# Performance work log

Measured on AMD Instinct MI355X. Metric: run time of the kernel, lower is better.

The kernel has to match this reference:

```python
import jax, jax.numpy as jnp
import numpy as np

B, S, D = 4, 2048, 1024

def setup_inputs() -> dict:
    key = jax.random.key(0)
    ks = jax.random.split(key, 7)
    s = 1.0 / np.sqrt(D)
    return {
        "x":  jax.random.normal(ks[0], (B, S, D), dtype=jnp.float32),
        "Wq": jax.random.uniform(ks[1], (D, D), jnp.float32, -s, s),
        "bq": jax.random.uniform(ks[2], (D,),  jnp.float32, -s, s),
        "Wk": jax.random.uniform(ks[3], (D, D), jnp.float32, -s, s),
        "bk": jax.random.uniform(ks[4], (D,),  jnp.float32, -s, s),
        "Wv": jax.random.uniform(ks[5], (D, D), jnp.float32, -s, s),
        "bv": jax.random.uniform(ks[6], (D,),  jnp.float32, -s, s),
    }

def reference(x, Wq, bq, Wk, bk, Wv, bv):
    # Q/K/V projections: [B,S,D]
    Q = jnp.einsum('bsd,de->bse', x, Wq) + bq
    K = jnp.einsum('bsd,de->bse', x, Wk) + bk
    V = jnp.einsum('bsd,de->bse', x, Wv) + bv
    scale = 1.0 / jnp.sqrt(jnp.asarray(K.shape[-1], K.dtype))
    scores = jnp.einsum('bqd,bkd->bqk', Q, K) * scale  # [B,S,S]
    weights = jax.nn.softmax(scores, axis=-1)
    return jnp.einsum('bqk,bkd->bqd', weights, V)
```

## Files before the change

### kernel.cpp

```cpp
#include <hip/hip_runtime.h>

typedef __attribute__((ext_vector_type(4))) float f32x4;
typedef __attribute__((ext_vector_type(8))) short bf16x8;

__device__ __forceinline__ float bf2f(unsigned short u) {
  union { unsigned int i; float f; } x; x.i = ((unsigned int)u) << 16; return x.f;
}
__device__ __forceinline__ unsigned short f2bf(float f) {
  union { float f; unsigned int i; } x; x.f = f;
  unsigned int r = (x.i + 0x7FFFu + ((x.i >> 16) & 1u)) >> 16;
  return (unsigned short)r;
}

#define BARX __builtin_amdgcn_s_barrier()
#define LGK0 asm volatile("s_waitcnt lgkmcnt(0)" ::: "memory")
#define GLD(gsrc, ldsoff)                                                        \
  __builtin_amdgcn_global_load_lds(                                              \
      (const __attribute__((address_space(1))) void*)(gsrc),                     \
      (__attribute__((address_space(3))) void*)&lds[ldsoff], 16, 0, 0)

__global__ __launch_bounds__(256) void cvt_f2b(const float* __restrict__ src,
                                               unsigned short* __restrict__ dst, long n4) {
  long i = (long)blockIdx.x * 256 + threadIdx.x;
  long stride = (long)gridDim.x * 256;
  for (; i < n4; i += stride) {
    float4 v = *(const float4*)&src[i * 4];
    ushort4 o;
    o.x = f2bf(v.x); o.y = f2bf(v.y); o.z = f2bf(v.z); o.w = f2bf(v.w);
    *(ushort4*)&dst[i * 4] = o;
  }
}

__global__ __launch_bounds__(256) void transpose_f2b(const float* __restrict__ src,
                                                     unsigned short* __restrict__ dst,
                                                     int rows, int cols) {
  __shared__ float t[32][33];
  int bx = blockIdx.x * 32, by = blockIdx.y * 32;
  int tx = threadIdx.x, ty = threadIdx.y;
#pragma unroll
  for (int k = 0; k < 4; ++k)
    t[ty + 8 * k][tx] = src[(long)(by + ty + 8 * k) * cols + bx + tx];
  __syncthreads();
#pragma unroll
  for (int k = 0; k < 4; ++k)
    dst[(long)(bx + ty + 8 * k) * rows + by + tx] = f2bf(t[tx][ty + 8 * k]);
}

__global__ __launch_bounds__(256) void transpose_v(const unsigned short* __restrict__ src,
                                                   unsigned short* __restrict__ dst) {
  __shared__ unsigned short t[32][33];
  const long sb = (long)blockIdx.z * 2048 * 3072;
  const long db = (long)blockIdx.z * 1024 * 2048;
  int bx = blockIdx.x * 32, by = blockIdx.y * 32;
  int tx = threadIdx.x, ty = threadIdx.y;
#pragma unroll
  for (int k = 0; k < 4; ++k)
    t[ty + 8 * k][tx] = src[sb + (long)(by + ty + 8 * k) * 3072 + bx + tx];
  __syncthreads();
#pragma unroll
  for (int k = 0; k < 4; ++k)
    dst[db + (long)(bx + ty + 8 * k) * 2048 + by + tx] = t[tx][ty + 8 * k];
}

template <int MODE>
__global__ __launch_bounds__(512, 2) void gemm4p(const unsigned short* __restrict__ Ap,
                                                 const unsigned short* __restrict__ Bp,
                                                 void* __restrict__ Cv,
                                                 const float* __restrict__ q_,
                                                 const float* __restrict__ k_,
                                                 const float* __restrict__ v_,
                                                 int Kd, int lda, int ldb, int ldc, float scale,
                                                 long sA, long sB, long sC) {
  __shared__ unsigned short lds[65536];
  const int bz = blockIdx.z;
  Ap += (long)bz * sA; Bp += (long)bz * sB;
  const int tid = threadIdx.x;
  const int m0 = blockIdx.x * 256, n0 = blockIdx.y * 256;
  const int lane = tid & 63, wave = tid >> 6;
  const int wm = wave >> 2, wn = wave & 3;
  const int rr = tid >> 3;
  const int cSrc = ((tid & 7) ^ (rr & 7)) << 3;
  const int lc = lane & 15, lr = lane >> 4;
  const int x0 = (lc & 4) << 3;
  const int x1 = 32 ^ x0;
  const int klo = (lr << 3) ^ ((lc & 3) << 3);
  const int aoff = (wm * 128 + lc) * 64 + klo;
  const int boff = 16384 + (wn * 64 + lc) * 64 + klo;
  const int NT = Kd >> 6;

#define ST4(bufo, reg0, half, P, R0, ld, k0s)                                                    \
  {                                                                                              \
    _Pragma("unroll") for (int i_ = 0; i_ < 2; ++i_) {                                           \
      const unsigned short* g_ =                                                                 \
          (P) + (long)((R0) + (half) * 128 + i_ * 64 + rr) * (ld) + ((k0s) + cSrc);              \
      GLD(g_, (bufo) + (reg0) + (half) * 8192 + i_ * 4096 + tid * 8);                            \
    }                                                                                            \
  }

  f32x4 acc[8][4] = {};

  ST4(0, 16384, 0, Bp, n0, ldb, 0); ST4(0, 16384, 1, Bp, n0, ldb, 0);
  ST4(0, 0, 0, Ap, m0, lda, 0);     ST4(0, 0, 1, Ap, m0, lda, 0);
  ST4(32768, 16384, 0, Bp, n0, ldb, 64); ST4(32768, 16384, 1, Bp, n0, ldb, 64);
  ST4(32768, 0, 0, Ap, m0, lda, 64);     ST4(32768, 0, 1, Ap, m0, lda, 64);
  asm volatile("s_waitcnt vmcnt(8)" ::: "memory");
  BARX;

  for (int t = 0; t < NT; ++t) {
    const int bufo = (t & 1) << 15;
    const unsigned short* Lp = &lds[bufo];
    const int kn = (t + 2) << 6;
    const bool pf = (t + 2 < NT);
    bf16x8 a0[4][2], a1[4][2], b0[2][2], b1[2][2];
#pragma unroll
    for (int mi = 0; mi < 4; ++mi) {
      a0[mi][0] = *(const bf16x8*)&Lp[aoff + mi * 1024 + x0];
      a0[mi][1] = *(const bf16x8*)&Lp[aoff + mi * 1024 + x1];
    }
#pragma unroll
    for (int ni = 0; ni < 2; ++ni) {
      b0[ni][0] = *(const bf16x8*)&Lp[boff + ni * 1024 + x0];
      b0[ni][1] = *(const bf16x8*)&Lp[boff + ni * 1024 + x1];
    }
    BARX; LGK0;
    __builtin_amdgcn_s_setprio(1);
#pragma unroll
    for (int mi = 0; mi < 4; ++mi)
#pragma unroll
      for (int ni = 0; ni < 2; ++ni)
#pragma unroll
        for (int x = 0; x < 2; ++x)
          acc[mi][ni] = __builtin_amdgcn_mfma_f32_16x16x32_bf16(a0[mi][x], b0[ni][x], acc[mi][ni], 0, 0, 0);
    __builtin_amdgcn_s_setprio(0);
    BARX;
#pragma unroll
    for (int ni = 0; ni < 2; ++ni) {
      b1[ni][0] = *(const bf16x8*)&Lp[boff + 2048 + ni * 1024 + x0];
      b1[ni][1] = *(const bf16x8*)&Lp[boff + 2048 + ni * 1024 + x1];
    }
    BARX; LGK0;
    __builtin_amdgcn_s_setprio(1);
#pragma unroll
    for (int mi = 0; mi < 4; ++mi)
#pragma unroll
      for (int ni = 0; ni < 2; ++ni)
#pragma unroll
        for (int x = 0; x < 2; ++x)
          acc[mi][2 + ni] = __builtin_amdgcn_mfma_f32_16x16x32_bf16(a0[mi][x], b1[ni][x], acc[mi][2 + ni], 0, 0, 0);
    __builtin_amdgcn_s_setprio(0);
    BARX;
#pragma unroll
    for (int mi = 0; mi < 4; ++mi) {
      a1[mi][0] = *(const bf16x8*)&Lp[aoff + 4096 + mi * 1024 + x0];
      a1[mi][1] = *(const bf16x8*)&Lp[aoff + 4096 + mi * 1024 + x1];
    }
    if (pf) ST4(bufo, 16384, 0, Bp, n0, ldb, kn);
    BARX; LGK0;
    __builtin_amdgcn_s_setprio(1);
#pragma unroll
    for (int mi = 0; mi < 4; ++mi)
#pragma unroll
      for (int ni = 0; ni < 2; ++ni)
#pragma unroll
        for (int x = 0; x < 2; ++x)
          acc[4 + mi][2 + ni] = __builtin_amdgcn_mfma_f32_16x16x32_bf16(a1[mi][x], b1[ni][x], acc[4 + mi][2 + ni], 0, 0, 0);
    __builtin_amdgcn_s_setprio(0);
    BARX;
    if (pf) {
      ST4(bufo, 16384, 1, Bp, n0, ldb, kn);
      ST4(bufo, 0, 0, Ap, m0, lda, kn);
      ST4(bufo, 0, 1, Ap, m0, lda, kn);
    }
    BARX; LGK0;
    __builtin_amdgcn_s_setprio(1);
#pragma unroll
    for (int mi = 0; mi < 4; ++mi)
#pragma unroll
      for (int ni = 0; ni < 2; ++ni)
#pragma unroll
        for (int x = 0; x < 2; ++x)
          acc[4 + mi][ni] = __builtin_amdgcn_mfma_f32_16x16x32_bf16(a1[mi][x], b0[ni][x], acc[4 + mi][ni], 0, 0, 0);
    __builtin_amdgcn_s_setprio(0);
    if (pf) { asm volatile("s_waitcnt vmcnt(8)" ::: "memory"); }
    else    { asm volatile("s_waitcnt vmcnt(0)" ::: "memory"); }
    BARX;
  }
#undef ST4

  const int r0 = m0 + wm * 128 + lr * 4;
  const int c0 = n0 + wn * 64 + lc;
  unsigned short* C = (unsigned short*)Cv + (long)bz * sC;
#pragma unroll
  for (int nh = 0; nh < 2; ++nh)
#pragma unroll
    for (int ni = 0; ni < 2; ++ni) {
      const int col = c0 + nh * 32 + ni * 16;
      float bv = 0.0f;
      if (MODE == 0)
        bv = (col < 1024) ? q_[col] : ((col < 2048) ? k_[col - 1024] : v_[col - 2048]);
#pragma unroll
      for (int mh = 0; mh < 2; ++mh)
#pragma unroll
        for (int mi = 0; mi < 4; ++mi)
#pragma unroll
          for (int r = 0; r < 4; ++r) {
            float val = acc[mh * 4 + mi][nh * 2 + ni][r];
            val = (MODE == 0) ? (val + bv) : __expf(val * scale);
            C[(long)(r0 + mh * 64 + mi * 16 + r) * ldc + col] = f2bf(val);
          }
    }
}

__global__ __launch_bounds__(512, 2) void gemmpv(const unsigned short* __restrict__ Av,
                                                 const unsigned short* __restrict__ Bv,
                                                 float* __restrict__ Out,
                                                 const float* __restrict__ invden,
                                                 int Kd, int lda, int ldb, int ldc,
                                                 long sA, long sB, long sC) {
  __shared__ unsigned short lds[73728];
  const int bz = blockIdx.z;
  Av += (long)bz * sA; Bv += (long)bz * sB;
  const int tid = threadIdx.x;
  const int m0 = blockIdx.x * 128, n0 = blockIdx.y * 256;
  const int lane = tid & 63, wave = tid >> 6;
  const int wm = wave >> 2, wn = wave & 3;
  const int rr = tid >> 3;
  const int cSrc = ((tid & 7) ^ (rr & 7)) << 3;
  const int lc = lane & 15, lr = lane >> 4;
  const int x0 = (lc & 4) << 3;
  const int x1 = 32 ^ x0;
  const int klo = (lr << 3) ^ ((lc & 3) << 3);
  const int aoff = (wm * 64 + lc) * 64 + klo;
  const int boff = 8192 + (wn * 64 + lc) * 64 + klo;
  const int NT = Kd >> 6;

#define STA_PV(bufo, k0s)                                                                        \
  {                                                                                              \
    _Pragma("unroll") for (int i_ = 0; i_ < 2; ++i_) {                                           \
      const unsigned short* g_ = Av + (long)(m0 + i_ * 64 + rr) * lda + ((k0s) + cSrc);          \
      GLD(g_, (bufo) + i_ * 4096 + tid * 8);                                                     \
    }                                                                                            \
  }
#define STB_PV(bufo, k0s)                                                                        \
  {                                                                                              \
    _Pragma("unroll") for (int i_ = 0; i_ < 4; ++i_) {                                           \
      const unsigned short* g_ = Bv + (long)(n0 + i_ * 64 + rr) * ldb + ((k0s) + cSrc);          \
      GLD(g_, (bufo) + 8192 + i_ * 4096 + tid * 8);                                              \
    }                                                                                            \
  }

  f32x4 acc[4][4] = {};

  STB_PV(0, 0);      STA_PV(0, 0);
  STB_PV(24576, 64); STA_PV(24576, 64);
  asm volatile("s_waitcnt vmcnt(6)" ::: "memory");
  BARX;

  int cur = 0;
  for (int t = 0; t < NT; ++t) {
    const int stg = (cur >= 1) ? cur - 1 : 2;
    const unsigned short* Lp = &lds[cur * 24576];
    const int so = stg * 24576;
    const int kn = (t + 2) << 6;
    const bool pf = (t + 2 < NT);
    bf16x8 a0[2][2], a1[2][2], bb[2][2][2];
#pragma unroll
    for (int nh = 0; nh < 2; ++nh)
#pragma unroll
      for (int ni = 0; ni < 2; ++ni) {
        bb[nh][ni][0] = *(const bf16x8*)&Lp[boff + nh * 2048 + ni * 1024 + x0];
        bb[nh][ni][1] = *(const bf16x8*)&Lp[boff + nh * 2048 + ni * 1024 + x1];
      }
#pragma unroll
    for (int mi = 0; mi < 2; ++mi) {
      a0[mi][0] = *(const bf16x8*)&Lp[aoff + mi * 1024 + x0];
      a0[mi][1] = *(const bf16x8*)&Lp[aoff + mi * 1024 + x1];
    }
    if (pf) STB_PV(so, kn);
    BARX; LGK0;
    __builtin_amdgcn_s_setprio(1);
#pragma unroll
    for (int mi = 0; mi < 2; ++mi)
#pragma unroll
      for (int nh = 0; nh < 2; ++nh)
#pragma unroll
        for (int ni = 0; ni < 2; ++ni)
#pragma unroll
          for (int x = 0; x < 2; ++x)
            acc[mi][nh * 2 + ni] = __builtin_amdgcn_mfma_f32_16x16x32_bf16(
                a0[mi][x], bb[nh][ni][x], acc[mi][nh * 2 + ni], 0, 0, 0);
    __builtin_amdgcn_s_setprio(0);
    BARX;
#pragma unroll
    for (int mi = 0; mi < 2; ++mi) {
      a1[mi][0] = *(const bf16x8*)&Lp[aoff + 2048 + mi * 1024 + x0];
      a1[mi][1] = *(const bf16x8*)&Lp[aoff + 2048 + mi * 1024 + x1];
    }
    if (pf) STA_PV(so, kn);
    BARX; LGK0;
    __builtin_amdgcn_s_setprio(1);
#pragma unroll
    for (int mi = 0; mi < 2; ++mi)
#pragma unroll
      for (int nh = 0; nh < 2; ++nh)
#pragma unroll
        for (int ni = 0; ni < 2; ++ni)
#pragma unroll
          for (int x = 0; x < 2; ++x)
            acc[2 + mi][nh * 2 + ni] = __builtin_amdgcn_mfma_f32_16x16x32_bf16(
                a1[mi][x], bb[nh][ni][x], acc[2 + mi][nh * 2 + ni], 0, 0, 0);
    __builtin_amdgcn_s_setprio(0);
    if (pf) { asm volatile("s_waitcnt vmcnt(6)" ::: "memory"); }
    else    { asm volatile("s_waitcnt vmcnt(0)" ::: "memory"); }
    BARX;
    cur = (cur == 2) ? 0 : cur + 1;
  }
#undef STA_PV
#undef STB_PV

  const int r0 = m0 + wm * 64 + lr * 4;
  const int c0 = n0 + wn * 64 + lc;
  float* O = Out + (long)bz * sC;
  const float* idn = invden + (long)bz * 2048;
  float iv[2][2][4];
#pragma unroll
  for (int mh = 0; mh < 2; ++mh)
#pragma unroll
    for (int mi = 0; mi < 2; ++mi)
#pragma unroll
      for (int r = 0; r < 4; ++r)
        iv[mh][mi][r] = idn[r0 + mh * 32 + mi * 16 + r];
#pragma unroll
  for (int mh = 0; mh < 2; ++mh)
#pragma unroll
    for (int mi = 0; mi < 2; ++mi)
#pragma unroll
      for (int r = 0; r < 4; ++r) {
        const int row = r0 + mh * 32 + mi * 16 + r;
#pragma unroll
        for (int nh = 0; nh < 2; ++nh)
#pragma unroll
          for (int ni = 0; ni < 2; ++ni)
            O[(long)row * ldc + (c0 + nh * 32 + ni * 16)] =
                acc[mh * 2 + mi][nh * 2 + ni][r] * iv[mh][mi][r];
      }
}

__global__ __launch_bounds__(256) void rowsum_inv(const unsigned short* __restrict__ E,
                                                  float* __restrict__ invden) {
  const long row = blockIdx.x;
  const unsigned short* p = E + row * 2048;
  const int tid = threadIdx.x;
  const int lane = tid & 63, wave = tid >> 6;
  ushort4 h0 = *(const ushort4*)&p[tid * 8];
  ushort4 h1 = *(const ushort4*)&p[tid * 8 + 4];
  float s = bf2f(h0.x) + bf2f(h0.y) + bf2f(h0.z) + bf2f(h0.w) +
            bf2f(h1.x) + bf2f(h1.y) + bf2f(h1.z) + bf2f(h1.w);
#pragma unroll
  for (int o = 32; o >= 1; o >>= 1) s += __shfl_xor(s, o);
  __shared__ float ss[4];
  if (lane == 0) ss[wave] = s;
  __syncthreads();
  if (tid == 0) invden[row] = 1.0f / (ss[0] + ss[1] + ss[2] + ss[3]);
}

extern "C" void kernel_launch(void* const* d_in, const int* in_sizes, int n_in,
                              void* d_out, int out_size, void* d_ws, size_t ws_size,
                              hipStream_t stream) {
  const float* x  = (const float*)d_in[0];
  const float* Wq = (const float*)d_in[1];
  const float* bq = (const float*)d_in[2];
  const float* Wk = (const float*)d_in[3];
  const float* bk = (const float*)d_in[4];
  const float* Wv = (const float*)d_in[5];
  const float* bv = (const float*)d_in[6];
  float* out = (float*)d_out;

  const int Bb = 4, S = 2048, D = 1024;
  const long MS = (long)Bb * S;

  char* ws = (char*)d_ws;
  unsigned short* xb  = (unsigned short*)(ws);
  unsigned short* Wt  = (unsigned short*)(ws + (16L << 20));
  unsigned short* QKV = (unsigned short*)(ws + (22L << 20));
  unsigned short* Sc  = (unsigned short*)(ws + (70L << 20));
  unsigned short* VT  = xb;
  float* invden = (float*)(ws + (16L << 20));

  cvt_f2b<<<2048, 256, 0, stream>>>(x, xb, MS * D / 4);

  dim3 tb(32, 8);
  dim3 tg(D / 32, D / 32);
  transpose_f2b<<<tg, tb, 0, stream>>>(Wq, Wt, D, D);
  transpose_f2b<<<tg, tb, 0, stream>>>(Wk, Wt + 1024 * 1024, D, D);
  transpose_f2b<<<tg, tb, 0, stream>>>(Wv, Wt + 2 * 1024 * 1024, D, D);

  dim3 pgrid(MS / 256, 3072 / 256, 1);
  gemm4p<0><<<pgrid, 512, 0, stream>>>(xb, Wt, QKV, bq, bk, bv, D, D, D, 3072, 1.0f, 0, 0, 0);

  dim3 vtg(D / 32, S / 32, Bb);
  transpose_v<<<vtg, tb, 0, stream>>>(QKV + 2048, VT);

  dim3 sgrid(S / 256, S / 256, Bb);
  gemm4p<1><<<sgrid, 512, 0, stream>>>(QKV, QKV + 1024, Sc, nullptr, nullptr, nullptr,
                                       D, 3072, 3072, S, 1.0f / 32.0f,
                                       (long)S * 3072, (long)S * 3072, (long)S * S);

  rowsum_inv<<<MS, 256, 0, stream>>>(Sc, invden);

  dim3 ogrid(S / 128, D / 256, Bb);
  gemmpv<<<ogrid, 512, 0, stream>>>(Sc, VT, out, invden, S, S, S, D,
                                    (long)S * S, (long)D * S, (long)S * D);
}
```

Baseline: 188.1 us.

## Unify all GEMMs onto 128x256 triple-buffered kernel with incremental load pointers

Removes the 256x256 double-buffered gemm4p kernel and routes the QKV projection and the QK^T score GEMM through the 128x256 three-stage pipelined kernel that the PV product already used, selected by a MODE template parameter. Global-load addresses are now precomputed per thread and advanced by 64 each K step, replacing per-iteration address recomputation. The change doubles the grid size for the first two GEMMs, which improves wave balance and latency hiding, but lowers per-block arithmetic intensity and reuse of the B operand.

```diff
diff --git a/kernel.cpp b/kernel.cpp
--- a/kernel.cpp
+++ b/kernel.cpp
@@ -63,163 +63,18 @@
 }
 
 template <int MODE>
-__global__ __launch_bounds__(512, 2) void gemm4p(const unsigned short* __restrict__ Ap,
+__global__ __launch_bounds__(512, 2) void gemm2p(const unsigned short* __restrict__ Ap,
                                                  const unsigned short* __restrict__ Bp,
                                                  void* __restrict__ Cv,
                                                  const float* __restrict__ q_,
                                                  const float* __restrict__ k_,
                                                  const float* __restrict__ v_,
+                                                 const float* __restrict__ invden,
                                                  int Kd, int lda, int ldb, int ldc, float scale,
-                                                 long sA, long sB, long sC) {
-  __shared__ unsigned short lds[65536];
-  const int bz = blockIdx.z;
-  Ap += (long)bz * sA; Bp += (long)bz * sB;
-  const int tid = threadIdx.x;
-  const int m0 = blockIdx.x * 256, n0 = blockIdx.y * 256;
-  const int lane = tid & 63, wave = tid >> 6;
-  const int wm = wave >> 2, wn = wave & 3;
-  const int rr = tid >> 3;
-  const int cSrc = ((tid & 7) ^ (rr & 7)) << 3;
-  const int lc = lane & 15, lr = lane >> 4;
-  const int x0 = (lc & 4) << 3;
-  const int x1 = 32 ^ x0;
-  const int klo = (lr << 3) ^ ((lc & 3) << 3);
-  const int aoff = (wm * 128 + lc) * 64 + klo;
-  const int boff = 16384 + (wn * 64 + lc) * 64 + klo;
-  const int NT = Kd >> 6;
-
-#define ST4(bufo, reg0, half, P, R0, ld, k0s)                                                    \
-  {                                                                                              \
-    _Pragma("unroll") for (int i_ = 0; i_ < 2; ++i_) {                                           \
-      const unsigned short* g_ =                                                                 \
-          (P) + (long)((R0) + (half) * 128 + i_ * 64 + rr) * (ld) + ((k0s) + cSrc);              \
-      GLD(g_, (bufo) + (reg0) + (half) * 8192 + i_ * 4096 + tid * 8);                            \
-    }                                                                                            \
-  }
-
-  f32x4 acc[8][4] = {};
-
-  ST4(0, 16384, 0, Bp, n0, ldb, 0); ST4(0, 16384, 1, Bp, n0, ldb, 0);
-  ST4(0, 0, 0, Ap, m0, lda, 0);     ST4(0, 0, 1, Ap, m0, lda, 0);
-  ST4(32768, 16384, 0, Bp, n0, ldb, 64); ST4(32768, 16384, 1, Bp, n0, ldb, 64);
-  ST4(32768, 0, 0, Ap, m0, lda, 64);     ST4(32768, 0, 1, Ap, m0, lda, 64);
-  asm volatile("s_waitcnt vmcnt(8)" ::: "memory");
-  BARX;
-
-  for (int t = 0; t < NT; ++t) {
-    const int bufo = (t & 1) << 15;
-    const unsigned short* Lp = &lds[bufo];
-    const int kn = (t + 2) << 6;
-    const bool pf = (t + 2 < NT);
-    bf16x8 a0[4][2], a1[4][2], b0[2][2], b1[2][2];
-#pragma unroll
-    for (int mi = 0; mi < 4; ++mi) {
-      a0[mi][0] = *(const bf16x8*)&Lp[aoff + mi * 1024 + x0];
-      a0[mi][1] = *(const bf16x8*)&Lp[aoff + mi * 1024 + x1];
-    }
-#pragma unroll
-    for (int ni = 0; ni < 2; ++ni) {
-      b0[ni][0] = *(const bf16x8*)&Lp[boff + ni * 1024 + x0];
-      b0[ni][1] = *(const bf16x8*)&Lp[boff + ni * 1024 + x1];
-    }
-    BARX; LGK0;
-    __builtin_amdgcn_s_setprio(1);
-#pragma unroll
-    for (int mi = 0; mi < 4; ++mi)
-#pragma unroll
-      for (int ni = 0; ni < 2; ++ni)
-#pragma unroll
-        for (int x = 0; x < 2; ++x)
-          acc[mi][ni] = __builtin_amdgcn_mfma_f32_16x16x32_bf16(a0[mi][x], b0[ni][x], acc[mi][ni], 0, 0, 0);
-    __builtin_amdgcn_s_setprio(0);
-    BARX;
-#pragma unroll
-    for (int ni = 0; ni < 2; ++ni) {
-      b1[ni][0] = *(const bf16x8*)&Lp[boff + 2048 + ni * 1024 + x0];
-      b1[ni][1] = *(const bf16x8*)&Lp[boff + 2048 + ni * 1024 + x1];
-    }
-    BARX; LGK0;
-    __builtin_amdgcn_s_setprio(1);
-#pragma unroll
-    for (int mi = 0; mi < 4; ++mi)
-#pragma unroll
-      for (int ni = 0; ni < 2; ++ni)
-#pragma unroll
-        for (int x = 0; x < 2; ++x)
-          acc[mi][2 + ni] = __builtin_amdgcn_mfma_f32_16x16x32_bf16(a0[mi][x], b1[ni][x], acc[mi][2 + ni], 0, 0, 0);
-    __builtin_amdgcn_s_setprio(0);
-    BARX;
-#pragma unroll
-    for (int mi = 0; mi < 4; ++mi) {
-      a1[mi][0] = *(const bf16x8*)&Lp[aoff + 4096 + mi * 1024 + x0];
-      a1[mi][1] = *(const bf16x8*)&Lp[aoff + 4096 + mi * 1024 + x1];
-    }
-    if (pf) ST4(bufo, 16384, 0, Bp, n0, ldb, kn);
-    BARX; LGK0;
-    __builtin_amdgcn_s_setprio(1);
-#pragma unroll
-    for (int mi = 0; mi < 4; ++mi)
-#pragma unroll
-      for (int ni = 0; ni < 2; ++ni)
-#pragma unroll
-        for (int x = 0; x < 2; ++x)
-          acc[4 + mi][2 + ni] = __builtin_amdgcn_mfma_f32_16x16x32_bf16(a1[mi][x], b1[ni][x], acc[4 + mi][2 + ni], 0, 0, 0);
-    __builtin_amdgcn_s_setprio(0);
-    BARX;
-    if (pf) {
-      ST4(bufo, 16384, 1, Bp, n0, ldb, kn);
-      ST4(bufo, 0, 0, Ap, m0, lda, kn);
-      ST4(bufo, 0, 1, Ap, m0, lda, kn);
-    }
-    BARX; LGK0;
-    __builtin_amdgcn_s_setprio(1);
-#pragma unroll
-    for (int mi = 0; mi < 4; ++mi)
-#pragma unroll
-      for (int ni = 0; ni < 2; ++ni)
-#pragma unroll
-        for (int x = 0; x < 2; ++x)
-          acc[4 + mi][ni] = __builtin_amdgcn_mfma_f32_16x16x32_bf16(a1[mi][x], b0[ni][x], acc[4 + mi][ni], 0, 0, 0);
-    __builtin_amdgcn_s_setprio(0);
-    if (pf) { asm volatile("s_waitcnt vmcnt(8)" ::: "memory"); }
-    else    { asm volatile("s_waitcnt vmcnt(0)" ::: "memory"); }
-    BARX;
-  }
-#undef ST4
-
-  const int r0 = m0 + wm * 128 + lr * 4;
-  const int c0 = n0 + wn * 64 + lc;
-  unsigned short* C = (unsigned short*)Cv + (long)bz * sC;
-#pragma unroll
-  for (int nh = 0; nh < 2; ++nh)
-#pragma unroll
-    for (int ni = 0; ni < 2; ++ni) {
-      const int col = c0 + nh * 32 + ni * 16;
-      float bv = 0.0f;
-      if (MODE == 0)
-        bv = (col < 1024) ? q_[col] : ((col < 2048) ? k_[col - 1024] : v_[col - 2048]);
-#pragma unroll
-      for (int mh = 0; mh < 2; ++mh)
-#pragma unroll
-        for (int mi = 0; mi < 4; ++mi)
-#pragma unroll
-          for (int r = 0; r < 4; ++r) {
-            float val = acc[mh * 4 + mi][nh * 2 + ni][r];
-            val = (MODE == 0) ? (val + bv) : __expf(val * scale);
-            C[(long)(r0 + mh * 64 + mi * 16 + r) * ldc + col] = f2bf(val);
-          }
-    }
-}
-
-__global__ __launch_bounds__(512, 2) void gemmpv(const unsigned short* __restrict__ Av,
-                                                 const unsigned short* __restrict__ Bv,
-                                                 float* __restrict__ Out,
-                                                 const float* __restrict__ invden,
-                                                 int Kd, int lda, int ldb, int ldc,
                                                  long sA, long sB, long sC) {
   __shared__ unsigned short lds[73728];
   const int bz = blockIdx.z;
-  Av += (long)bz * sA; Bv += (long)bz * sB;
+  Ap += (long)bz * sA; Bp += (long)bz * sB;
   const int tid = threadIdx.x;
   const int m0 = blockIdx.x * 128, n0 = blockIdx.y * 256;
   const int lane = tid & 63, wave = tid >> 6;
@@ -234,25 +89,24 @@
   const int boff = 8192 + (wn * 64 + lc) * 64 + klo;
   const int NT = Kd >> 6;
 
-#define STA_PV(bufo, k0s)                                                                        \
-  {                                                                                              \
-    _Pragma("unroll") for (int i_ = 0; i_ < 2; ++i_) {                                           \
-      const unsigned short* g_ = Av + (long)(m0 + i_ * 64 + rr) * lda + ((k0s) + cSrc);          \
-      GLD(g_, (bufo) + i_ * 4096 + tid * 8);                                                     \
-    }                                                                                            \
-  }
-#define STB_PV(bufo, k0s)                                                                        \
-  {                                                                                              \
-    _Pragma("unroll") for (int i_ = 0; i_ < 4; ++i_) {                                           \
-      const unsigned short* g_ = Bv + (long)(n0 + i_ * 64 + rr) * ldb + ((k0s) + cSrc);          \
-      GLD(g_, (bufo) + 8192 + i_ * 4096 + tid * 8);                                              \
-    }                                                                                            \
-  }
+  const unsigned short* pA0 = Ap + (long)(m0 + rr) * lda + cSrc;
+  const unsigned short* pA1 = pA0 + (long)64 * lda;
+  const unsigned short* pB0 = Bp + (long)(n0 + rr) * ldb + cSrc;
+  const unsigned short* pB1 = pB0 + (long)64 * ldb;
+  const unsigned short* pB2 = pB0 + (long)128 * ldb;
+  const unsigned short* pB3 = pB0 + (long)192 * ldb;
+  const int dA0 = tid * 8, dA1 = 4096 + tid * 8;
+  const int dB0 = 8192 + tid * 8, dB1 = 12288 + tid * 8;
+  const int dB2 = 16384 + tid * 8, dB3 = 20480 + tid * 8;
+#define STAGE6(so)                                                                \
+  { GLD(pB0, (so) + dB0); GLD(pB1, (so) + dB1); GLD(pA0, (so) + dA0);             \
+    GLD(pB2, (so) + dB2); GLD(pB3, (so) + dB3); GLD(pA1, (so) + dA1); }
+#define ADV { pA0 += 64; pA1 += 64; pB0 += 64; pB1 += 64; pB2 += 64; pB3 += 64; }
 
   f32x4 acc[4][4] = {};
 
-  STB_PV(0, 0);      STA_PV(0, 0);
-  STB_PV(24576, 64); STA_PV(24576, 64);
+  STAGE6(0); ADV;
+  STAGE6(24576); ADV;
   asm volatile("s_waitcnt vmcnt(6)" ::: "memory");
   BARX;
 
@@ -261,7 +115,6 @@
     const int stg = (cur >= 1) ? cur - 1 : 2;
     const unsigned short* Lp = &lds[cur * 24576];
     const int so = stg * 24576;
-    const int kn = (t + 2) << 6;
     const bool pf = (t + 2 < NT);
     bf16x8 a0[2][2], a1[2][2], bb[2][2][2];
 #pragma unroll
@@ -276,7 +129,7 @@
       a0[mi][0] = *(const bf16x8*)&Lp[aoff + mi * 1024 + x0];
       a0[mi][1] = *(const bf16x8*)&Lp[aoff + mi * 1024 + x1];
     }
-    if (pf) STB_PV(so, kn);
+    if (pf) { GLD(pB0, so + dB0); GLD(pB1, so + dB1); GLD(pA0, so + dA0); }
     BARX; LGK0;
     __builtin_amdgcn_s_setprio(1);
 #pragma unroll
@@ -296,7 +149,7 @@
       a1[mi][0] = *(const bf16x8*)&Lp[aoff + 2048 + mi * 1024 + x0];
       a1[mi][1] = *(const bf16x8*)&Lp[aoff + 2048 + mi * 1024 + x1];
     }
-    if (pf) STA_PV(so, kn);
+    if (pf) { GLD(pB2, so + dB2); GLD(pB3, so + dB3); GLD(pA1, so + dA1); }
     BARX; LGK0;
     __builtin_amdgcn_s_setprio(1);
 #pragma unroll
@@ -314,36 +167,48 @@
     else    { asm volatile("s_waitcnt vmcnt(0)" ::: "memory"); }
     BARX;
     cur = (cur == 2) ? 0 : cur + 1;
+    ADV;
   }
-#undef STA_PV
-#undef STB_PV
+#undef STAGE6
+#undef ADV
 
   const int r0 = m0 + wm * 64 + lr * 4;
   const int c0 = n0 + wn * 64 + lc;
-  float* O = Out + (long)bz * sC;
-  const float* idn = invden + (long)bz * 2048;
-  float iv[2][2][4];
-#pragma unroll
-  for (int mh = 0; mh < 2; ++mh)
-#pragma unroll
-    for (int mi = 0; mi < 2; ++mi)
-#pragma unroll
-      for (int r = 0; r < 4; ++r)
-        iv[mh][mi][r] = idn[r0 + mh * 32 + mi * 16 + r];
-#pragma unroll
-  for (int mh = 0; mh < 2; ++mh)
-#pragma unroll
-    for (int mi = 0; mi < 2; ++mi)
+  if (MODE == 2) {
+    float* O = (float*)Cv + (long)bz * sC;
+    const float* idn = invden + (long)bz * 2048;
+#pragma unroll
+    for (int j = 0; j < 4; ++j)
 #pragma unroll
       for (int r = 0; r < 4; ++r) {
-        const int row = r0 + mh * 32 + mi * 16 + r;
+        const int row = r0 + j * 16 + r;
+        const float iv = idn[row];
 #pragma unroll
         for (int nh = 0; nh < 2; ++nh)
 #pragma unroll
           for (int ni = 0; ni < 2; ++ni)
-            O[(long)row * ldc + (c0 + nh * 32 + ni * 16)] =
-                acc[mh * 2 + mi][nh * 2 + ni][r] * iv[mh][mi][r];
+            O[(long)row * ldc + (c0 + nh * 32 + ni * 16)] = acc[j][nh * 2 + ni][r] * iv;
       }
+  } else {
+    unsigned short* C = (unsigned short*)Cv + (long)bz * sC;
+#pragma unroll
+    for (int nh = 0; nh < 2; ++nh)
+#pragma unroll
+      for (int ni = 0; ni < 2; ++ni) {
+        const int col = c0 + nh * 32 + ni * 16;
+        float bv = 0.0f;
+        if (MODE == 0)
+          bv = (col < 1024) ? q_[col] : ((col < 2048) ? k_[col - 1024] : v_[col - 2048]);
+#pragma unroll
+        for (int j = 0; j < 4; ++j)
+#pragma unroll
+          for (int r = 0; r < 4; ++r) {
+            float val = acc[j][nh * 2 + ni][r];
+            val = (MODE == 0) ? (val + bv) : __expf(val * scale);
+            C[(long)(r0 + j * 16 + r) * ldc + col] = f2bf(val);
+          }
+      }
+  }
 }
 
 __global__ __launch_bounds__(256) void rowsum_inv(const unsigned short* __restrict__ E,
@@ -395,20 +260,22 @@
   transpose_f2b<<<tg, tb, 0, stream>>>(Wk, Wt + 1024 * 1024, D, D);
   transpose_f2b<<<tg, tb, 0, stream>>>(Wv, Wt + 2 * 1024 * 1024, D, D);
 
-  dim3 pgrid(MS / 256, 3072 / 256, 1);
-  gemm4p<0><<<pgrid, 512, 0, stream>>>(xb, Wt, QKV, bq, bk, bv, D, D, D, 3072, 1.0f, 0, 0, 0);
+  dim3 pgrid(MS / 128, 3072 / 256, 1);
+  gemm2p<0><<<pgrid, 512, 0, stream>>>(xb, Wt, QKV, bq, bk, bv, nullptr,
+                                       D, D, D, 3072, 1.0f, 0, 0, 0);
 
   dim3 vtg(D / 32, S / 32, Bb);
   transpose_v<<<vtg, tb, 0, stream>>>(QKV + 2048, VT);
 
-  dim3 sgrid(S / 256, S / 256, Bb);
-  gemm4p<1><<<sgrid, 512, 0, stream>>>(QKV, QKV + 1024, Sc, nullptr, nullptr, nullptr,
+  dim3 sgrid(S / 128, S / 256, Bb);
+  gemm2p<1><<<sgrid, 512, 0, stream>>>(QKV, QKV + 1024, Sc, nullptr, nullptr, nullptr, nullptr,
                                        D, 3072, 3072, S, 1.0f / 32.0f,
                                        (long)S * 3072, (long)S * 3072, (long)S * S);
 
   rowsum_inv<<<MS, 256, 0, stream>>>(Sc, invden);
 
   dim3 ogrid(S / 128, D / 256, Bb);
-  gemmpv<<<ogrid, 512, 0, stream>>>(Sc, VT, out, invden, S, S, S, D,
-                                    (long)S * S, (long)D * S, (long)S * D);
-}
+  gemm2p<2><<<ogrid, 512, 0, stream>>>(Sc, VT, out, nullptr, nullptr, nullptr, invden,
+                                       S, S, S, D, 1.0f,
+                                       (long)S * S, (long)D * S, (long)S * D);
+}
```

New measurement: 180.6 us. -4.0%, faster.
